# Performance work log

Hardware: AMD Instinct MI355X
Metric: run time of the kernel (lower is better)

## Reference

```python
import jax, jax.numpy as jnp
import numpy as np

B, T, IN, H, L, OUT = 64, 512, 128, 512, 2, 1


def setup_inputs() -> dict:
    key = jax.random.key(0)
    ks = jax.random.split(key, 4 * L + 3)
    inp = {"X": jax.random.normal(ks[0], (B, T, IN), dtype=jnp.float32)}
    s_in = 1.0 / np.sqrt(H)
    for l in range(L):
        d_in = IN if l == 0 else H
        inp[f"W_ih{l}"] = jax.random.uniform(ks[1 + 4 * l], (3 * H, d_in), minval=-s_in, maxval=s_in, dtype=jnp.float32)
        inp[f"W_hh{l}"] = jax.random.uniform(ks[2 + 4 * l], (3 * H, H), minval=-s_in, maxval=s_in, dtype=jnp.float32)
        inp[f"b_ih{l}"] = jax.random.uniform(ks[3 + 4 * l], (3 * H,), minval=-s_in, maxval=s_in, dtype=jnp.float32)
        inp[f"b_hh{l}"] = jax.random.uniform(ks[4 + 4 * l], (3 * H,), minval=-s_in, maxval=s_in, dtype=jnp.float32)
    s_fc = 1.0 / np.sqrt(H)
    inp["fc_W"] = jax.random.uniform(ks[-2], (OUT, H), minval=-s_fc, maxval=s_fc, dtype=jnp.float32)
    inp["fc_b"] = jax.random.uniform(ks[-1], (OUT,), minval=-s_fc, maxval=s_fc, dtype=jnp.float32)
    return inp


def _gru_layer(x_seq, W_ih, W_hh, b_ih, b_hh):
    # x_seq: [B, T, D_in] -> hidden sequence [B, T, H]
    # Precompute input projections for all timesteps (one big GEMM).
    xg = jnp.einsum('btd,gd->btg', x_seq, W_ih) + b_ih  # [B, T, 3H]
    h0 = jnp.zeros((x_seq.shape[0], W_hh.shape[1]), dtype=x_seq.dtype)

    def step(h, xt):
        hg = h @ W_hh.T + b_hh  # [B, 3H]
        xr, xz, xn = jnp.split(xt, 3, axis=-1)
        hr, hz, hn = jnp.split(hg, 3, axis=-1)
        r = jax.nn.sigmoid(xr + hr)
        z = jax.nn.sigmoid(xz + hz)
        n = jnp.tanh(xn + r * hn)
        h_new = (1.0 - z) * n + z * h
        return h_new, h_new

    _, hs = jax.lax.scan(step, h0, xg.transpose(1, 0, 2))  # hs: [T, B, H]
    return hs.transpose(1, 0, 2)


def reference(X, W_ih0, W_hh0, b_ih0, b_hh0, W_ih1, W_hh1, b_ih1, b_hh1, fc_W, fc_b):
    h = _gru_layer(X, W_ih0, W_hh0, b_ih0, b_hh0)
    h = _gru_layer(h, W_ih1, W_hh1, b_ih1, b_hh1)
    return h[:, -1, :] @ fc_W.T + fc_b  # [B, OUT]
```

## Files before the change

kernel.cpp:

```cpp
#include <hip/hip_runtime.h>


constexpr int Bb = 64, Tt = 512, DIN = 128, Hh = 512;
constexpr int BH = Bb * Hh;
constexpr int S0 = 644;
constexpr int S1 = 1028;
constexpr int PR = 17;

typedef float  f32x4  __attribute__((ext_vector_type(4)));
typedef short  bf16x8 __attribute__((ext_vector_type(8)));
typedef int    i32x4  __attribute__((ext_vector_type(4)));
typedef unsigned long long u64;

#define MFMA16 __builtin_amdgcn_mfma_f32_16x16x32_bf16

__device__ __forceinline__ unsigned rne_bf16(unsigned xb){
    return (xb + 0x7FFFu + ((xb >> 16) & 1u)) >> 16;
}
__device__ __forceinline__ unsigned pack_split(float x){
    unsigned hb = rne_bf16(__float_as_uint(x));
    float hf = __uint_as_float(hb << 16);
    unsigned lb = rne_bf16(__float_as_uint(x - hf));
    return (hb << 16) | lb;
}
__device__ __forceinline__ float unpack_f32(unsigned u){
    return __uint_as_float(u & 0xFFFF0000u) + __uint_as_float(u << 16);
}

union FragU { unsigned w[4]; bf16x8 v; };

__device__ __forceinline__ void make_wfrag(const float* p, bf16x8& wh, bf16x8& wl){
    FragU hi, lo;
#pragma unroll
    for (int i = 0; i < 4; ++i){
        unsigned pa = pack_split(p[2*i]), pb = pack_split(p[2*i+1]);
        hi.w[i] = (pa >> 16) | (pb & 0xFFFF0000u);
        lo.w[i] = (pa & 0xFFFFu) | (pb << 16);
    }
    wh = hi.v; wl = lo.v;
}
__device__ __forceinline__ void make_afrag(const unsigned* u, bf16x8& ah, bf16x8& al){
    FragU hi, lo;
#pragma unroll
    for (int i = 0; i < 4; ++i){
        unsigned a = u[2*i], b = u[2*i+1];
        hi.w[i] = (a >> 16) | (b & 0xFFFF0000u);
        lo.w[i] = (a & 0xFFFFu) | (b << 16);
    }
    ah = hi.v; al = lo.v;
}

__device__ __forceinline__ u64 ald64(const u64* p){
    return __hip_atomic_load(p, __ATOMIC_RELAXED, __HIP_MEMORY_SCOPE_AGENT);
}
__device__ __forceinline__ void ast64(u64* p, u64 v){
    __hip_atomic_store(p, v, __ATOMIC_RELAXED, __HIP_MEMORY_SCOPE_AGENT);
}

__device__ __forceinline__ bool bad4(const i32x4& v, unsigned tag){
    unsigned x = ((unsigned)v[0] ^ tag) | ((unsigned)v[1] ^ tag)
               | ((unsigned)v[2] ^ tag) | ((unsigned)v[3] ^ tag);
    return (x & 1u) != 0u;
}
__device__ __forceinline__ void fix4(const unsigned* p, unsigned tag, i32x4& v){
    if (bad4(v, tag)){
        for (;;){
            u64 a = ald64((const u64*)p);
            u64 b = ald64((const u64*)p + 1);
            v[0] = (int)(unsigned)a; v[1] = (int)(unsigned)(a >> 32);
            v[2] = (int)(unsigned)b; v[3] = (int)(unsigned)(b >> 32);
            if (!bad4(v, tag)) break;
            __builtin_amdgcn_s_sleep(1);
        }
    }
}

template<bool BIG>
__global__ __launch_bounds__(512, 1) void gru_main(
    const float* __restrict__ X,
    const float* __restrict__ Wih0, const float* __restrict__ Whh0,
    const float* __restrict__ bih0, const float* __restrict__ bhh0,
    const float* __restrict__ Wih1, const float* __restrict__ Whh1,
    const float* __restrict__ bih1, const float* __restrict__ bhh1,
    const float* __restrict__ fcW, const float* __restrict__ fcb,
    float* __restrict__ out,
    unsigned* hseq0, unsigned* hseq1)
{
    __builtin_amdgcn_fence(__ATOMIC_ACQUIRE, "agent");

    __shared__ unsigned Alds[16 * S1];
    __shared__ float P[8][3][16 * PR];
    __shared__ unsigned hout[256];

    const int tid  = threadIdx.x;
    const int lane = tid & 63;
    const int w    = tid >> 6;
    const bool isL1 = blockIdx.x >= 128;
    const int lb = isL1 ? (int)blockIdx.x - 128 : (int)blockIdx.x;
    const int m  = lb >> 5;
    const int cb = lb & 31;
    const int c0 = cb * 16;
    const int STR  = isL1 ? S1 : S0;
    const int HOFF = isL1 ? 512 : 128;

    const bool active = isL1 || (w < 5);

    bf16x8 whi[4][3], wlo[4][3];
    if (active){
        const int n = lane & 15;
#pragma unroll
        for (int ks = 0; ks < 4; ++ks){
            int kq = w * 128 + ks * 32 + (lane >> 4) * 8;
            const float* src; long kloc, rowlen;
            if (isL1){
                if (kq < 512){ src = Wih1; kloc = kq; } else { src = Whh1; kloc = kq - 512; }
                rowlen = 512;
            } else {
                if (kq < 128){ src = Wih0; kloc = kq; rowlen = 128; }
                else         { src = Whh0; kloc = kq - 128; rowlen = 512; }
            }
#pragma unroll
            for (int g = 0; g < 3; ++g){
                long row = (long)g * Hh + c0 + n;
                make_wfrag(src + row * rowlen + kloc, whi[ks][g], wlo[ks][g]);
            }
        }
    }
    float Br = 0.f, Bz = 0.f, Bin = 0.f, Bhn = 0.f;
    if (tid < 256){
        int c = c0 + (tid & 15);
        const float* bi = isL1 ? bih1 : bih0;
        const float* bh = isL1 ? bhh1 : bhh0;
        Br  = bi[c] + bh[c];
        Bz  = bi[Hh + c] + bh[Hh + c];
        Bin = bi[2*Hh + c];
        Bhn = bh[2*Hh + c];
    }

    for (int t = 0; t < Tt; ++t){
        if (isL1){
            const unsigned* s0 = hseq0 + ((long)t * Bb + m*16) * (long)Hh;
            long r1 = BIG ? (long)(t-1) * BH : (long)((t-1) & 1) * BH;
            const unsigned* s1 = hseq1 + r1 + (long)(m*16) * Hh;
            unsigned tag1 = BIG ? 1u : (1u - (((unsigned)(t-1) >> 1) & 1u));
            const unsigned* a0[4]; const unsigned* a1[4];
            i32x4 v0[4], v1[4];
#pragma unroll
            for (int it = 0; it < 4; ++it){
                int j = it*512 + tid; int row = j >> 7, col = (j & 127) * 4;
                a0[it] = s0 + (long)row * Hh + col;
                v0[it] = *(const i32x4*)a0[it];
            }
            if (t > 0){
#pragma unroll
                for (int it = 0; it < 4; ++it){
                    int j = it*512 + tid; int row = j >> 7, col = (j & 127) * 4;
                    a1[it] = s1 + (long)row * Hh + col;
                    v1[it] = *(const i32x4*)a1[it];
                }
            }
#pragma unroll
            for (int it = 0; it < 4; ++it) fix4(a0[it], 1u, v0[it]);
            if (t > 0){
#pragma unroll
                for (int it = 0; it < 4; ++it) fix4(a1[it], tag1, v1[it]);
            } else {
#pragma unroll
                for (int it = 0; it < 4; ++it) v1[it] = i32x4{0,0,0,0};
            }
#pragma unroll
            for (int it = 0; it < 4; ++it){
                int j = it*512 + tid; int row = j >> 7, col = (j & 127) * 4;
                *(i32x4*)(Alds + row * S1 + col) = v0[it];
                *(i32x4*)(Alds + row * S1 + 512 + col) = v1[it];
            }
        } else {
            {
                int row = tid >> 5, c4 = (tid & 31) * 4;
                f32x4 xv = *(const f32x4*)(X + ((long)(m*16 + row) * Tt + t) * DIN + c4);
                i32x4 pv;
                pv[0] = (int)pack_split(xv[0]);
                pv[1] = (int)pack_split(xv[1]);
                pv[2] = (int)pack_split(xv[2]);
                pv[3] = (int)pack_split(xv[3]);
                *(i32x4*)(Alds + row * S0 + c4) = pv;
            }
            if (t > 0){
                const unsigned* s0 = hseq0 + ((long)(t-1) * Bb + m*16) * (long)Hh;
                const unsigned* a0[4]; i32x4 v0[4];
#pragma unroll
                for (int it = 0; it < 4; ++it){
                    int j = it*512 + tid; int row = j >> 7, col = (j & 127) * 4;
                    a0[it] = s0 + (long)row * Hh + col;
                    v0[it] = *(const i32x4*)a0[it];
                }
#pragma unroll
                for (int it = 0; it < 4; ++it) fix4(a0[it], 1u, v0[it]);
#pragma unroll
                for (int it = 0; it < 4; ++it){
                    int j = it*512 + tid; int row = j >> 7, col = (j & 127) * 4;
                    *(i32x4*)(Alds + row * S0 + 128 + col) = v0[it];
                }
            } else {
#pragma unroll
                for (int it = 0; it < 8; ++it){
                    int j = it*512 + tid;
                    *(u64*)(Alds + (j >> 8) * S0 + 128 + (j & 255) * 2) = 0ULL;
                }
            }
        }
        __syncthreads();

        if (active){
            f32x4 a0 = {0.f,0.f,0.f,0.f}, a1 = a0, a2 = a0;
            const unsigned* arow = Alds + (lane & 15) * STR + w * 128 + (lane >> 4) * 8;
#pragma unroll
            for (int ks = 0; ks < 4; ++ks){
                unsigned uu[8];
                *(i32x4*)&uu[0] = *(const i32x4*)(arow + ks*32);
                *(i32x4*)&uu[4] = *(const i32x4*)(arow + ks*32 + 4);
                bf16x8 ah, al; make_afrag(uu, ah, al);
                a0 = MFMA16(ah, whi[ks][0], a0, 0,0,0);
                a0 = MFMA16(ah, wlo[ks][0], a0, 0,0,0);
                a0 = MFMA16(al, whi[ks][0], a0, 0,0,0);
                a1 = MFMA16(ah, whi[ks][1], a1, 0,0,0);
                a1 = MFMA16(ah, wlo[ks][1], a1, 0,0,0);
                a1 = MFMA16(al, whi[ks][1], a1, 0,0,0);
                a2 = MFMA16(ah, whi[ks][2], a2, 0,0,0);
                a2 = MFMA16(ah, wlo[ks][2], a2, 0,0,0);
                a2 = MFMA16(al, whi[ks][2], a2, 0,0,0);
            }
            int q = lane >> 4, n = lane & 15;
#pragma unroll
            for (int r4 = 0; r4 < 4; ++r4){
                int idx = (q*4 + r4)*PR + n;
                P[w][0][idx] = a0[r4];
                P[w][1][idx] = a1[r4];
                P[w][2][idx] = a2[r4];
            }
        }
        __syncthreads();

        unsigned wtag = isL1 ? (BIG ? 1u : (1u - (((unsigned)t >> 1) & 1u))) : 1u;
        if (tid < 256){
            int bm = tid >> 4, n = tid & 15;
            int idx = bm * PR + n;
            float sr, sz, snx, snh;
            if (isL1){
                sr  = P[0][0][idx]+P[1][0][idx]+P[2][0][idx]+P[3][0][idx]
                    + P[4][0][idx]+P[5][0][idx]+P[6][0][idx]+P[7][0][idx];
                sz  = P[0][1][idx]+P[1][1][idx]+P[2][1][idx]+P[3][1][idx]
                    + P[4][1][idx]+P[5][1][idx]+P[6][1][idx]+P[7][1][idx];
                snx = P[0][2][idx]+P[1][2][idx]+P[2][2][idx]+P[3][2][idx];
                snh = P[4][2][idx]+P[5][2][idx]+P[6][2][idx]+P[7][2][idx];
            } else {
                sr  = P[0][0][idx]+P[1][0][idx]+P[2][0][idx]+P[3][0][idx]+P[4][0][idx];
                sz  = P[0][1][idx]+P[1][1][idx]+P[2][1][idx]+P[3][1][idx]+P[4][1][idx];
                snx = P[0][2][idx];
                snh = P[1][2][idx]+P[2][2][idx]+P[3][2][idx]+P[4][2][idx];
            }
            float r  = 1.f/(1.f + __expf(-(sr + Br)));
            float z  = 1.f/(1.f + __expf(-(sz + Bz)));
            float ee = __expf(2.f*(snx + Bin + r*(snh + Bhn)));
            float nn = 1.f - 2.f/(ee + 1.f);
            float hp = unpack_f32(Alds[bm*STR + HOFF + c0 + n]);
            float hnew = (1.f - z)*nn + z*hp;
            hout[tid] = (pack_split(hnew) & ~1u) | wtag;
        }
        __syncthreads();

        if (tid < 128){
            int bm = tid >> 3, k = (tid & 7) * 2;
            u64 v = (u64)hout[bm*16 + k] | ((u64)hout[bm*16 + k + 1] << 32);
            unsigned* base = isL1
                ? hseq1 + (BIG ? (long)t * BH : (long)(t & 1) * BH)
                : hseq0 + (long)t * BH;
            ast64((u64*)(base + (long)(m*16 + bm) * Hh + c0 + k), v);
        }
    }

    if (isL1 && cb == 31){
        unsigned ftag = BIG ? 1u : (1u - (((unsigned)(Tt-1) >> 1) & 1u));
        const unsigned* hb = hseq1 + (BIG ? (long)(Tt-1) * BH : (long)((Tt-1) & 1) * BH);
        int half = lane >> 5, l5 = lane & 31;
        int b = m*16 + w*2 + half;
        const u64* hrow = (const u64*)(hb + (long)b * Hh);
        float p = 0.f;
#pragma unroll
        for (int i = 0; i < 8; ++i){
            int k = l5 + 32*i;
            u64 v = ald64(hrow + k);
            while (((((unsigned)v ^ ftag) | ((unsigned)(v >> 32) ^ ftag)) & 1u) != 0u){
                __builtin_amdgcn_s_sleep(1);
                v = ald64(hrow + k);
            }
            p += unpack_f32((unsigned)v) * fcW[2*k]
               + unpack_f32((unsigned)(v >> 32)) * fcW[2*k+1];
        }
#pragma unroll
        for (int off = 16; off > 0; off >>= 1) p += __shfl_xor(p, off);
        if (l5 == 0) out[b] = p + fcb[0];
    }
}

extern "C" void kernel_launch(void* const* d_in, const int* in_sizes, int n_in,
                              void* d_out, int out_size, void* d_ws, size_t ws_size,
                              hipStream_t stream) {
    const float* X    = (const float*)d_in[0];
    const float* Wih0 = (const float*)d_in[1];
    const float* Whh0 = (const float*)d_in[2];
    const float* bih0 = (const float*)d_in[3];
    const float* bhh0 = (const float*)d_in[4];
    const float* Wih1 = (const float*)d_in[5];
    const float* Whh1 = (const float*)d_in[6];
    const float* bih1 = (const float*)d_in[7];
    const float* bhh1 = (const float*)d_in[8];
    const float* fcW  = (const float*)d_in[9];
    const float* fcb  = (const float*)d_in[10];
    float* out = (float*)d_out;

    unsigned* hseq0 = (unsigned*)d_ws;
    unsigned* hseq1 = hseq0 + (long)Tt * BH;
    size_t need_big = (size_t)2 * Tt * BH * 4;
    bool big = ws_size >= need_big;

    if (big)
        gru_main<true><<<256, 512, 0, stream>>>(X, Wih0, Whh0, bih0, bhh0,
                                                Wih1, Whh1, bih1, bhh1, fcW, fcb,
                                                out, hseq0, hseq1);
    else
        gru_main<false><<<256, 512, 0, stream>>>(X, Wih0, Whh0, bih0, bhh0,
                                                 Wih1, Whh1, bih1, bhh1, fcW, fcb,
                                                 out, hseq0, hseq1);
}
```

Before: 1.734 ms.

## Store hidden state directly from gate threads and refine cross-block polling

Each gate thread now writes its packed hidden value straight to the global sequence buffer instead of staging through shared memory and a second 64-bit store pass. Removing that pass drops a barrier-dependent step from every timestep. Polling on stale data now first retries with sc0 vector loads before falling back to atomic loads. Block-to-layer/batch mapping is interleaved so layer-0 and layer-1 blocks alternate across CUs. Each value is stored twice (a plain store then an atomic), which adds store traffic, and the polling relies on inline-asm cache semantics.

```diff
diff --git a/kernel.cpp b/kernel.cpp
--- a/kernel.cpp
+++ b/kernel.cpp
@@ -53,8 +53,18 @@
 __device__ __forceinline__ u64 ald64(const u64* p){
     return __hip_atomic_load(p, __ATOMIC_RELAXED, __HIP_MEMORY_SCOPE_AGENT);
 }
-__device__ __forceinline__ void ast64(u64* p, u64 v){
+__device__ __forceinline__ void ast32(unsigned* p, unsigned v){
     __hip_atomic_store(p, v, __ATOMIC_RELAXED, __HIP_MEMORY_SCOPE_AGENT);
+}
+
+__device__ __forceinline__ i32x4 ld_sc0(const unsigned* p){
+    i32x4 v;
+    asm volatile("global_load_dwordx4 %0, %1, off sc0\n\ts_waitcnt vmcnt(0)"
+                 : "=v"(v) : "v"(p) : "memory");
+    return v;
+}
+__device__ __forceinline__ void st_plain(unsigned* p, unsigned v){
+    asm volatile("global_store_dword %0, %1, off" :: "v"(p), "v"(v) : "memory");
 }
 
 __device__ __forceinline__ bool bad4(const i32x4& v, unsigned tag){
@@ -63,15 +73,20 @@
     return (x & 1u) != 0u;
 }
 __device__ __forceinline__ void fix4(const unsigned* p, unsigned tag, i32x4& v){
-    if (bad4(v, tag)){
-        for (;;){
-            u64 a = ald64((const u64*)p);
-            u64 b = ald64((const u64*)p + 1);
-            v[0] = (int)(unsigned)a; v[1] = (int)(unsigned)(a >> 32);
-            v[2] = (int)(unsigned)b; v[3] = (int)(unsigned)(b >> 32);
-            if (!bad4(v, tag)) break;
-            __builtin_amdgcn_s_sleep(1);
-        }
+    if (!bad4(v, tag)) return;
+#pragma unroll 1
+    for (int i = 0; i < 6; ++i){
+        v = ld_sc0(p);
+        if (!bad4(v, tag)) return;
+        __builtin_amdgcn_s_sleep(1);
+    }
+    for (;;){
+        u64 a = ald64((const u64*)p);
+        u64 b = ald64((const u64*)p + 1);
+        v[0] = (int)(unsigned)a; v[1] = (int)(unsigned)(a >> 32);
+        v[2] = (int)(unsigned)b; v[3] = (int)(unsigned)(b >> 32);
+        if (!bad4(v, tag)) return;
+        __builtin_amdgcn_s_sleep(2);
     }
 }
 
@@ -90,15 +105,14 @@
 
     __shared__ unsigned Alds[16 * S1];
     __shared__ float P[8][3][16 * PR];
-    __shared__ unsigned hout[256];
 
     const int tid  = threadIdx.x;
     const int lane = tid & 63;
     const int w    = tid >> 6;
-    const bool isL1 = blockIdx.x >= 128;
-    const int lb = isL1 ? (int)blockIdx.x - 128 : (int)blockIdx.x;
-    const int m  = lb >> 5;
-    const int cb = lb & 31;
+    const int g    = (int)blockIdx.x & 7;
+    const bool isL1 = g >= 4;
+    const int m  = g & 3;
+    const int cb = (int)blockIdx.x >> 3;
     const int c0 = cb * 16;
     const int STR  = isL1 ? S1 : S0;
     const int HOFF = isL1 ? 512 : 128;
@@ -120,9 +134,9 @@
                 else         { src = Whh0; kloc = kq - 128; rowlen = 512; }
             }
 #pragma unroll
-            for (int g = 0; g < 3; ++g){
-                long row = (long)g * Hh + c0 + n;
-                make_wfrag(src + row * rowlen + kloc, whi[ks][g], wlo[ks][g]);
+            for (int gg = 0; gg < 3; ++gg){
+                long row = (long)gg * Hh + c0 + n;
+                make_wfrag(src + row * rowlen + kloc, whi[ks][gg], wlo[ks][gg]);
             }
         }
     }
@@ -265,18 +279,15 @@
             float nn = 1.f - 2.f/(ee + 1.f);
             float hp = unpack_f32(Alds[bm*STR + HOFF + c0 + n]);
             float hnew = (1.f - z)*nn + z*hp;
-            hout[tid] = (pack_split(hnew) & ~1u) | wtag;
+            unsigned pk = (pack_split(hnew) & ~1u) | wtag;
+            unsigned* dst = isL1
+                ? hseq1 + (BIG ? (long)t * BH : (long)(t & 1) * BH)
+                        + (long)(m*16 + bm) * Hh + c0 + n
+                : hseq0 + ((long)t * Bb + m*16 + bm) * (long)Hh + c0 + n;
+            st_plain(dst, pk);
+            ast32(dst, pk);
         }
         __syncthreads();
-
-        if (tid < 128){
-            int bm = tid >> 3, k = (tid & 7) * 2;
-            u64 v = (u64)hout[bm*16 + k] | ((u64)hout[bm*16 + k + 1] << 32);
-            unsigned* base = isL1
-                ? hseq1 + (BIG ? (long)t * BH : (long)(t & 1) * BH)
-                : hseq0 + (long)t * BH;
-            ast64((u64*)(base + (long)(m*16 + bm) * Hh + c0 + k), v);
-        }
     }
 
     if (isL1 && cb == 31){
@@ -284,18 +295,16 @@
         const unsigned* hb = hseq1 + (BIG ? (long)(Tt-1) * BH : (long)((Tt-1) & 1) * BH);
         int half = lane >> 5, l5 = lane & 31;
         int b = m*16 + w*2 + half;
-        const u64* hrow = (const u64*)(hb + (long)b * Hh);
+        const unsigned* hrow = hb + (long)b * Hh;
         float p = 0.f;
 #pragma unroll
-        for (int i = 0; i < 8; ++i){
-            int k = l5 + 32*i;
-            u64 v = ald64(hrow + k);
-            while (((((unsigned)v ^ ftag) | ((unsigned)(v >> 32) ^ ftag)) & 1u) != 0u){
-                __builtin_amdgcn_s_sleep(1);
-                v = ald64(hrow + k);
-            }
-            p += unpack_f32((unsigned)v) * fcW[2*k]
-               + unpack_f32((unsigned)(v >> 32)) * fcW[2*k+1];
+        for (int cch = 0; cch < 4; ++cch){
+            int col = (l5 + 32*cch) * 4;
+            i32x4 v = *(const i32x4*)(hrow + col);
+            fix4(hrow + col, ftag, v);
+#pragma unroll
+            for (int jj = 0; jj < 4; ++jj)
+                p += unpack_f32((unsigned)v[jj]) * fcW[col + jj];
         }
 #pragma unroll
         for (int off = 16; off > 0; off >>= 1) p += __shfl_xor(p, off);
```

After: 2.325 ms. 1.34x slower.
